# Performance work log

Hardware: AMD Instinct MI355X
Metric: run time of the kernel (lower is better)

Reference implementation:

```python
import jax, jax.numpy as jnp
import numpy as np

EPS = 1e-5
N_HEADS = 16
D_NOPE = 128
D_ROPE = 64
D_QK = D_NOPE + D_ROPE  # 192
D_V = 128
KV_RANK = 512
SCALE = D_QK ** -0.5


def rms_norm(x, w, eps=EPS):
    return x * jax.lax.rsqrt(jnp.mean(x * x, axis=-1, keepdims=True) + eps) * w


def apply_rope(x, c, s):
    # x: [..., D_ROPE], c/s broadcastable [..., D_ROPE//2]; half-split rotation
    x0, x1 = x[..., : D_ROPE // 2], x[..., D_ROPE // 2 :]
    return jnp.concatenate([x0 * c - x1 * s, x0 * s + x1 * c], axis=-1)


def setup_inputs() -> dict:
    key = jax.random.key(0)
    ks = jax.random.split(key, 8)
    B, S, H_DIM = 2, 2048, 2048
    Q_RANK = 1536
    w = lambda k, shp: jax.random.normal(k, shp, dtype=jnp.float32) * 0.02
    # real RoPE tables: [max_seq, D_ROPE//2]
    inv_freq = 1.0 / (10000.0 ** (np.arange(0, D_ROPE, 2, dtype=np.float32) / D_ROPE))
    ang = np.arange(S, dtype=np.float32)[:, None] * inv_freq[None, :]
    return {
        "x": jax.random.normal(ks[0], (B, S, H_DIM), dtype=jnp.float32),
        "positions": jnp.arange(S, dtype=jnp.int64),
        "Wqa": w(ks[1], (H_DIM, Q_RANK)),
        "g_qa": jnp.ones((Q_RANK,), jnp.float32),
        "Wqb": w(ks[2], (Q_RANK, N_HEADS * D_QK)),
        "Wkva": w(ks[3], (H_DIM, KV_RANK + D_ROPE)),
        "g_kva": jnp.ones((KV_RANK,), jnp.float32),
        "Wkvb": w(ks[4], (KV_RANK, N_HEADS * (D_NOPE + D_V))),
        "Wo": w(ks[5], (N_HEADS * D_V, H_DIM)),
        "cos": jnp.asarray(np.cos(ang)),
        "sin": jnp.asarray(np.sin(ang)),
    }


def reference(x, positions, Wqa, g_qa, Wqb, Wkva, g_kva, Wkvb, Wo, cos, sin):
    B, S, _ = x.shape
    # Q path: low-rank down, RMSNorm, up
    q = rms_norm(x @ Wqa, g_qa) @ Wqb  # [B,S,H*D_QK]
    q = q.reshape(B, S, N_HEADS, D_QK)
    q_nope, q_rope = q[..., :D_NOPE], q[..., D_NOPE:]
    c = cos[positions]  # [S, D_ROPE//2]
    s = sin[positions]
    q_rope = apply_rope(q_rope, c[None, :, None, :], s[None, :, None, :])
    # KV path: joint down-proj, split latent / rope-key
    kv_a = x @ Wkva  # [B,S,KV_RANK+D_ROPE]
    kv_latent = rms_norm(kv_a[..., :KV_RANK], g_kva)
    k_rope = apply_rope(kv_a[..., KV_RANK:], c[None, :, :], s[None, :, :])  # [B,S,D_ROPE]
    # up-project latent to per-head k_nope and v
    kv_b = (kv_latent @ Wkvb).reshape(B, S, N_HEADS, D_NOPE + D_V)
    k_nope, v = kv_b[..., :D_NOPE], kv_b[..., D_NOPE:]
    k = jnp.concatenate(
        [k_nope, jnp.broadcast_to(k_rope[:, :, None, :], (B, S, N_HEADS, D_ROPE))], axis=-1
    )  # [B,S,H,D_QK]
    q_full = jnp.concatenate([q_nope, q_rope], axis=-1)  # [B,S,H,D_QK]
    # causal SDPA with d_qk != d_v
    scores = jnp.einsum("bqhd,bkhd->bhqk", q_full, k) * SCALE
    causal = jnp.tril(jnp.ones((S, S), dtype=bool))
    scores = jnp.where(causal[None, None, :, :], scores, -jnp.inf)
    p = jax.nn.softmax(scores, axis=-1)
    out = jnp.einsum("bhqk,bkhd->bqhd", p, v).reshape(B, S, N_HEADS * D_V)
    return out @ Wo
```

## Files before the change

kernel.cpp:

```cpp
#include <hip/hip_runtime.h>
#include <hip/hip_bf16.h>

typedef __bf16 bf16;
typedef __bf16 bf16x8 __attribute__((ext_vector_type(8)));
typedef __bf16 bf16x4 __attribute__((ext_vector_type(4)));
typedef float f32x4 __attribute__((ext_vector_type(4)));

#define B_    2
#define S_    2048
#define HD    2048
#define NH    16
#define DQK   192
#define DV    128
#define QR    1536
#define KVR   512
#define NTOK  4096
#define NKVB  4096
#define NQB   3072
#define NQKVA 2176

#define EXP2F(x) __builtin_amdgcn_exp2f(x)

static __device__ __forceinline__ void gload16(const void* g, void* l) {
  __builtin_amdgcn_global_load_lds(
      (const __attribute__((address_space(1))) void*)g,
      (__attribute__((address_space(3))) void*)l, 16, 0, 0);
}

__global__ __launch_bounds__(256) void cvt_bf16(const float* __restrict__ in,
                                                bf16* __restrict__ out, long n) {
  long i = ((long)blockIdx.x * 256 + threadIdx.x) * 4;
  if (i + 3 < n) {
    float4 v = *(const float4*)(in + i);
    bf16x4 o = {(bf16)v.x, (bf16)v.y, (bf16)v.z, (bf16)v.w};
    *(bf16x4*)(out + i) = o;
  }
}

struct TransArgs {
  const float *s0, *s1, *s2, *s3, *s4;
  bf16 *d0, *d1, *d2, *d3, *d4;
};
__global__ __launch_bounds__(256) void transpose_all(TransArgs a) {
  __shared__ float tile[32][33];
  int bid = blockIdx.x;
  int seg, rel;
  if      (bid < 3072)  { seg = 0; rel = bid; }
  else if (bid < 4352)  { seg = 1; rel = bid - 3072; }
  else if (bid < 8960)  { seg = 2; rel = bid - 4352; }
  else if (bid < 11008) { seg = 3; rel = bid - 8960; }
  else                  { seg = 4; rel = bid - 11008; }
  const float* in = seg == 0 ? a.s0 : seg == 1 ? a.s1 : seg == 2 ? a.s2 : seg == 3 ? a.s3 : a.s4;
  bf16* out       = seg == 0 ? a.d0 : seg == 1 ? a.d1 : seg == 2 ? a.d2 : seg == 3 ? a.d3 : a.d4;
  int R   = seg == 0 ? 2048 : seg == 1 ? 2048 : seg == 2 ? 1536 : seg == 3 ? 512 : 2048;
  int C   = seg == 0 ? 1536 : seg == 1 ? 576  : seg == 2 ? 3072 : seg == 3 ? 4096 : 2048;
  int Np  = seg == 0 ? 1536 : seg == 1 ? 640  : seg == 2 ? 3072 : seg == 3 ? 4096 : 2048;
  int nbx = seg == 0 ? 48   : seg == 1 ? 20   : seg == 2 ? 96   : seg == 3 ? 128 : 64;
  int c0 = (rel % nbx) * 32;
  int r0 = (rel / nbx) * 32;
  int tx = threadIdx.x & 31, ty = threadIdx.x >> 5;
#pragma unroll
  for (int i = 0; i < 4; ++i) {
    int r = r0 + ty + i * 8, c = c0 + tx;
    tile[ty + i * 8][tx] = (c < C) ? in[(long)r * C + c] : 0.f;
  }
  __syncthreads();
#pragma unroll
  for (int i = 0; i < 4; ++i) {
    int oc = c0 + ty + i * 8;
    if (oc < Np) out[(long)oc * R + r0 + tx] = (bf16)tile[tx][ty + i * 8];
  }
}

#define GEMM_CORE(A, Bt, K)                                                    \
  __shared__ bf16 As[128 * 64];                                                \
  __shared__ bf16 Bs[128 * 64];                                                \
  const int t = threadIdx.x;                                                   \
  const int l = t & 63;                                                        \
  const int w = t >> 6;                                                        \
  const int m0 = blockIdx.y * 128;                                             \
  const int n0 = blockIdx.x * 128;                                             \
  const int wr = (w >> 1) * 64;                                                \
  const int wc = (w & 1) * 64;                                                 \
  const int lr = l & 15;                                                       \
  const int lg = l >> 4;                                                       \
  f32x4 acc[4][4] = {};                                                        \
  for (int k0 = 0; k0 < (K); k0 += 64) {                                       \
    __syncthreads();                                                           \
    _Pragma("unroll")                                                          \
    for (int j = 0; j < 4; ++j) {                                              \
      int s = j * 256 + t;                                                     \
      int row = s >> 3, sc = s & 7;                                            \
      int c = sc ^ (row & 7);                                                  \
      gload16((A) + (long)(m0 + row) * (K) + k0 + c * 8,                       \
              As + (j * 256 + w * 64) * 8);                                    \
      gload16((Bt) + (long)(n0 + row) * (K) + k0 + c * 8,                      \
              Bs + (j * 256 + w * 64) * 8);                                    \
    }                                                                          \
    __syncthreads();                                                           \
    _Pragma("unroll")                                                          \
    for (int kh = 0; kh < 2; ++kh) {                                           \
      bf16x8 af[4], bfr[4];                                                    \
      _Pragma("unroll")                                                        \
      for (int m = 0; m < 4; ++m) {                                            \
        int row = wr + m * 16 + lr;                                            \
        af[m] = *(const bf16x8*)(As + row * 64 + (((kh * 4 + lg) ^ (row & 7)) << 3)); \
      }                                                                        \
      _Pragma("unroll")                                                        \
      for (int n = 0; n < 4; ++n) {                                            \
        int row = wc + n * 16 + lr;                                            \
        bfr[n] = *(const bf16x8*)(Bs + row * 64 + (((kh * 4 + lg) ^ (row & 7)) << 3)); \
      }                                                                        \
      _Pragma("unroll")                                                        \
      for (int m = 0; m < 4; ++m)                                              \
        _Pragma("unroll")                                                      \
        for (int n = 0; n < 4; ++n)                                            \
          acc[m][n] = __builtin_amdgcn_mfma_f32_16x16x32_bf16(af[m], bfr[n], acc[m][n], 0, 0, 0); \
    }                                                                          \
  }

template <typename CT>
__global__ __launch_bounds__(256) void gemm_bf16(const bf16* __restrict__ A,
                                                 const bf16* __restrict__ Bt,
                                                 CT* __restrict__ C,
                                                 int M, int N, int K) {
  GEMM_CORE(A, Bt, K)
#pragma unroll
  for (int m = 0; m < 4; ++m)
#pragma unroll
    for (int n = 0; n < 4; ++n)
#pragma unroll
      for (int v = 0; v < 4; ++v) {
        int row = m0 + wr + m * 16 + lg * 4 + v;
        int col = n0 + wc + n * 16 + lr;
        C[(long)row * N + col] = (CT)acc[m][n][v];
      }
}

__global__ __launch_bounds__(256) void gemm_qf(const bf16* __restrict__ A,
                                               const bf16* __restrict__ Bt,
                                               const int* __restrict__ pos,
                                               const float* __restrict__ cosT,
                                               const float* __restrict__ sinT,
                                               bf16* __restrict__ q_bhsd) {
  const float SCALE = 0.07216878364870323f * 1.4426950408889634f;
  GEMM_CORE(A, Bt, QR)
  int c0 = n0 + wc;
  int h = c0 / 192;
  int part = c0 - h * 192;
#pragma unroll
  for (int m = 0; m < 4; ++m)
#pragma unroll
    for (int v = 0; v < 4; ++v) {
      int row = m0 + wr + m * 16 + lg * 4 + v;
      int b = row >> 11, s = row & (S_ - 1);
      long base = ((long)(b * NH + h) * S_ + s) * DQK;
      if (part < 128) {
#pragma unroll
        for (int n = 0; n < 4; ++n)
          q_bhsd[base + part + n * 16 + lr] = (bf16)(acc[m][n][v] * SCALE);
      } else {
        int p = pos[s] & (S_ - 1);
        float c_lo = cosT[p * 32 + lr],      s_lo = sinT[p * 32 + lr];
        float c_hi = cosT[p * 32 + 16 + lr], s_hi = sinT[p * 32 + 16 + lr];
        float o0 = acc[m][0][v] * c_lo - acc[m][2][v] * s_lo;
        float o1 = acc[m][1][v] * c_hi - acc[m][3][v] * s_hi;
        float o2 = acc[m][0][v] * s_lo + acc[m][2][v] * c_lo;
        float o3 = acc[m][1][v] * s_hi + acc[m][3][v] * c_hi;
        q_bhsd[base + 128 + lr] = (bf16)(o0 * SCALE);
        q_bhsd[base + 144 + lr] = (bf16)(o1 * SCALE);
        q_bhsd[base + 160 + lr] = (bf16)(o2 * SCALE);
        q_bhsd[base + 176 + lr] = (bf16)(o3 * SCALE);
      }
    }
}

__global__ __launch_bounds__(256) void gemm_kvb(const bf16* __restrict__ A,
                                                const bf16* __restrict__ Bt,
                                                bf16* __restrict__ k_bhsd,
                                                bf16* __restrict__ v_t) {
  GEMM_CORE(A, Bt, KVR)
  int c0 = n0 + wc;
  int h = c0 >> 8;
  int dbase = c0 & 64;
  bool vpart = (c0 >> 7) & 1;
  if (!vpart) {
#pragma unroll
    for (int m = 0; m < 4; ++m)
#pragma unroll
      for (int v = 0; v < 4; ++v) {
        int row = m0 + wr + m * 16 + lg * 4 + v;
        int b = row >> 11, s = row & (S_ - 1);
        long base = ((long)(b * NH + h) * S_ + s) * DQK + dbase;
#pragma unroll
        for (int n = 0; n < 4; ++n)
          k_bhsd[base + n * 16 + lr] = (bf16)acc[m][n][v];
      }
  } else {
#pragma unroll
    for (int m = 0; m < 4; ++m) {
      int row0 = m0 + wr + m * 16 + lg * 4;
      int b = row0 >> 11, s = row0 & (S_ - 1);
#pragma unroll
      for (int n = 0; n < 4; ++n) {
        int d = dbase + n * 16 + lr;
        bf16x4 o = {(bf16)acc[m][n][0], (bf16)acc[m][n][1],
                    (bf16)acc[m][n][2], (bf16)acc[m][n][3]};
        *(bf16x4*)(v_t + ((long)(b * NH + h) * DV + d) * S_ + s) = o;
      }
    }
  }
}

__global__ __launch_bounds__(256) void norm_prep(const bf16* __restrict__ xa,
                                                 const float* __restrict__ g_qa,
                                                 const float* __restrict__ g_kva,
                                                 const int* __restrict__ pos,
                                                 const float* __restrict__ cosT,
                                                 const float* __restrict__ sinT,
                                                 bf16* __restrict__ q_n,
                                                 bf16* __restrict__ kv_l,
                                                 bf16* __restrict__ k_bhsd) {
  int row = blockIdx.x;
  int t = threadIdx.x;
  int b = row >> 11, s = row & (S_ - 1);
  const bf16* xr = xa + (long)row * NQKVA;
  __shared__ float red[3];
  __shared__ bf16 rope_s[64];
  float vf[8];
  if (t < 192) {
    bf16x8 vv = *(const bf16x8*)(xr + t * 8);
    float ss = 0.f;
#pragma unroll
    for (int e = 0; e < 8; ++e) { vf[e] = (float)vv[e]; ss += vf[e] * vf[e]; }
#pragma unroll
    for (int m = 1; m < 64; m <<= 1) ss += __shfl_xor(ss, m);
    if ((t & 63) == 0) red[t >> 6] = ss;
  } else {
    int tt = t - 192;
    const bf16* xl = xr + QR;
    bf16x8 vv = *(const bf16x8*)(xl + tt * 8);
    float ss = 0.f;
#pragma unroll
    for (int e = 0; e < 8; ++e) { vf[e] = (float)vv[e]; ss += vf[e] * vf[e]; }
#pragma unroll
    for (int m = 1; m < 64; m <<= 1) ss += __shfl_xor(ss, m);
    float rs = rsqrtf(ss / KVR + 1e-5f);
    bf16x8 o;
#pragma unroll
    for (int e = 0; e < 8; ++e) o[e] = (bf16)(vf[e] * rs * g_kva[tt * 8 + e]);
    *(bf16x8*)(kv_l + (long)row * KVR + tt * 8) = o;
    if (tt < 32) {
      int p = pos[s] & (S_ - 1);
      float c = cosT[p * 32 + tt], sn = sinT[p * 32 + tt];
      float x0 = (float)xl[512 + tt], x1 = (float)xl[544 + tt];
      rope_s[tt] = (bf16)(x0 * c - x1 * sn);
      rope_s[32 + tt] = (bf16)(x0 * sn + x1 * c);
    }
  }
  __syncthreads();
  if (t < 192) {
    float ss = red[0] + red[1] + red[2];
    float rs = rsqrtf(ss / QR + 1e-5f);
    bf16x8 o;
#pragma unroll
    for (int e = 0; e < 8; ++e) o[e] = (bf16)(vf[e] * rs * g_qa[t * 8 + e]);
    *(bf16x8*)(q_n + (long)row * QR + t * 8) = o;
  } else {
    int tt = t - 192;
    bf16x8 rv = *(const bf16x8*)&rope_s[(tt & 7) * 8];
    long base0 = ((long)(b * NH + (tt >> 3)) * S_ + s) * DQK + 128 + (tt & 7) * 8;
    long base1 = ((long)(b * NH + 8 + (tt >> 3)) * S_ + s) * DQK + 128 + (tt & 7) * 8;
    *(bf16x8*)(k_bhsd + base0) = rv;
    *(bf16x8*)(k_bhsd + base1) = rv;
  }
}

#define KVB  64
#define DVP  144
__global__ __launch_bounds__(512) void flash4(const bf16* __restrict__ q_bhsd,
                                              const bf16* __restrict__ k_bhsd,
                                              const bf16* __restrict__ v_t,
                                              bf16* __restrict__ att) {
  __shared__ bf16 Ks[KVB * DQK];
  __shared__ bf16 Vs[DVP * KVB];
  __shared__ bf16 Ps[8][16 * 72];
  int bid = blockIdx.x;
  int bh = bid & 31;
  int qt = 15 - (bid >> 5);
  int b = bh >> 4, h = bh & 15;
  int q0 = qt * 128;
  int t = threadIdx.x;
  int w = t >> 6, l = t & 63;
  int lr = l & 15, lg = l >> 4;
  int qw = q0 + w * 16;

  const bf16* Qb = q_bhsd + (long)bh * S_ * DQK;
  const bf16* Kb = k_bhsd + (long)bh * S_ * DQK;
  const bf16* Vb = v_t + (long)bh * DV * S_;

  if (t < 128) {
    int rr = 128 + (t >> 3), cc = (t & 7) * 8;
    bf16 val = (bf16)((rr == 128) ? 1.0f : 0.0f);
    bf16x8 vvv = {val, val, val, val, val, val, val, val};
    *(bf16x8*)(Vs + rr * KVB + cc) = vvv;
  }

  bf16x8 qf[6];
#pragma unroll
  for (int t6 = 0; t6 < 6; ++t6)
    qf[t6] = *(const bf16x8*)(Qb + (long)(qw + lr) * DQK + t6 * 32 + lg * 8);

  f32x4 oacc[9] = {};
  float mrow[4] = {-1e30f, -1e30f, -1e30f, -1e30f};
  const int lr7 = lr & 7;

  int nkt = 2 * qt + 2;
  for (int kt = 0; kt < nkt; ++kt) {
    int k0 = kt * KVB;
    __syncthreads();
#pragma unroll
    for (int j = 0; j < 3; ++j) {
      int s = j * 512 + t;
      int r = s / 24, c1 = s - r * 24;
      int c = c1 ^ (r & 7);
      gload16(Kb + (long)(k0 + r) * DQK + c * 8, Ks + (j * 512 + w * 64) * 8);
    }
#pragma unroll
    for (int j = 0; j < 2; ++j) {
      int s = j * 512 + t;
      int d = s >> 3, c1 = s & 7;
      int c = c1 ^ (d & 7);
      gload16(Vb + (long)d * S_ + k0 + c * 8, Vs + (j * 512 + w * 64) * 8);
    }
    __syncthreads();
    if (k0 > qw + 15) continue;

    f32x4 sacc[4] = {};
#pragma unroll
    for (int n = 0; n < 4; ++n) {
      int rk = n * 16 + lr;
#pragma unroll
      for (int t6 = 0; t6 < 6; ++t6) {
        bf16x8 kf = *(const bf16x8*)(Ks + rk * DQK + (((t6 * 4 + lg) ^ lr7) << 3));
        sacc[n] = __builtin_amdgcn_mfma_f32_16x16x32_bf16(qf[t6], kf, sacc[n], 0, 0, 0);
      }
    }
    if (k0 + KVB - 1 > qw) {
#pragma unroll
      for (int n = 0; n < 4; ++n)
#pragma unroll
        for (int v = 0; v < 4; ++v) {
          int r = lg * 4 + v, c = n * 16 + lr;
          if (k0 + c > qw + r) sacc[n][v] = -1e30f;
        }
    }
    float mv[4];
#pragma unroll
    for (int v = 0; v < 4; ++v) {
      mv[v] = fmaxf(fmaxf(sacc[0][v], sacc[1][v]), fmaxf(sacc[2][v], sacc[3][v]));
#pragma unroll
      for (int msk = 1; msk < 16; msk <<= 1) mv[v] = fmaxf(mv[v], __shfl_xor(mv[v], msk));
    }
    bool grow = (mv[0] > mrow[0] + 8.f) | (mv[1] > mrow[1] + 8.f) |
                (mv[2] > mrow[2] + 8.f) | (mv[3] > mrow[3] + 8.f);
    if (__any(grow)) {
      float corr[4];
#pragma unroll
      for (int v = 0; v < 4; ++v) {
        float mt = fmaxf(mrow[v], mv[v]);
        corr[v] = EXP2F(mrow[v] - mt);
        mrow[v] = mt;
      }
#pragma unroll
      for (int dn = 0; dn < 9; ++dn)
#pragma unroll
        for (int v = 0; v < 4; ++v) oacc[dn][v] *= corr[v];
    }
#pragma unroll
    for (int v = 0; v < 4; ++v)
#pragma unroll
      for (int n = 0; n < 4; ++n)
        Ps[w][(lg * 4 + v) * 72 + n * 16 + lr] = (bf16)EXP2F(sacc[n][v] - mrow[v]);
#pragma unroll
    for (int kc = 0; kc < 2; ++kc) {
      bf16x8 pf = *(const bf16x8*)(Ps[w] + lr * 72 + kc * 32 + lg * 8);
#pragma unroll
      for (int dn = 0; dn < 9; ++dn) {
        int d = dn * 16 + lr;
        bf16x8 vf = *(const bf16x8*)(Vs + d * KVB + (((kc * 4 + lg) ^ lr7) << 3));
        oacc[dn] = __builtin_amdgcn_mfma_f32_16x16x32_bf16(pf, vf, oacc[dn], 0, 0, 0);
      }
    }
  }
  float rl[4];
#pragma unroll
  for (int v = 0; v < 4; ++v) {
    float lv = __shfl(oacc[8][v], lg * 16);
    rl[v] = 1.0f / lv;
  }
#pragma unroll
  for (int dn = 0; dn < 8; ++dn)
#pragma unroll
    for (int v = 0; v < 4; ++v) {
      int r = lg * 4 + v;
      float o = oacc[dn][v] * rl[v];
      att[((long)(b * S_ + qw + r)) * 2048 + h * 128 + dn * 16 + lr] = (bf16)o;
    }
}

extern "C" void kernel_launch(void* const* d_in, const int* in_sizes, int n_in,
                              void* d_out, int out_size, void* d_ws, size_t ws_size,
                              hipStream_t stream) {
  const float* x        = (const float*)d_in[0];
  const int* pos        = (const int*)d_in[1];
  const float* Wqa      = (const float*)d_in[2];
  const float* g_qa     = (const float*)d_in[3];
  const float* Wqb      = (const float*)d_in[4];
  const float* Wkva     = (const float*)d_in[5];
  const float* g_kva    = (const float*)d_in[6];
  const float* Wkvb     = (const float*)d_in[7];
  const float* Wo       = (const float*)d_in[8];
  const float* cosT     = (const float*)d_in[9];
  const float* sinT     = (const float*)d_in[10];
  float* out            = (float*)d_out;

  size_t off = 0;
  char* wsp = (char*)d_ws;
  auto alloc = [&](size_t n) { void* p = wsp + off; off += (n + 255) & ~(size_t)255; return p; };
  bf16*  Wqa_t  = (bf16*) alloc((size_t)QR * HD * 2);
  bf16*  Wkva_t = (bf16*) alloc((size_t)640 * HD * 2);
  bf16*  Wqb_t  = (bf16*) alloc((size_t)NQB * QR * 2);
  bf16*  Wkvb_t = (bf16*) alloc((size_t)NKVB * KVR * 2);
  bf16*  Wo_t   = (bf16*) alloc((size_t)HD * HD * 2);
  bf16*  x_bf   = (bf16*) alloc((size_t)NTOK * HD * 2);
  bf16*  q_bhsd = (bf16*) alloc((size_t)B_ * NH * S_ * DQK * 2);
  bf16*  k_bhsd = (bf16*) alloc((size_t)B_ * NH * S_ * DQK * 2);
  bf16*  v_t    = (bf16*) alloc((size_t)B_ * NH * DV * S_ * 2);
  bf16*  att    = (bf16*) alloc((size_t)NTOK * 2048 * 2);
  char*  T      = (char*) alloc((size_t)33554432);
  bf16*  xa  = (bf16*)T;
  bf16*  q_n = (bf16*)(T + 18874368);
  bf16*  kv_l = (bf16*)(T + 18874368 + 12582912);
  if (ws_size < off) return;

  cvt_bf16<<<(NTOK * HD / 4 + 255) / 256, 256, 0, stream>>>(x, x_bf, (long)NTOK * HD);
  TransArgs ta = {Wqa, Wkva, Wqb, Wkvb, Wo, Wqa_t, Wkva_t, Wqb_t, Wkvb_t, Wo_t};
  transpose_all<<<15104, 256, 0, stream>>>(ta);
  gemm_bf16<bf16><<<dim3(NQKVA / 128, NTOK / 128), 256, 0, stream>>>(x_bf, Wqa_t, xa, NTOK, NQKVA, HD);
  norm_prep<<<NTOK, 256, 0, stream>>>(xa, g_qa, g_kva, pos, cosT, sinT, q_n, kv_l, k_bhsd);
  gemm_qf<<<dim3(NQB / 128, NTOK / 128), 256, 0, stream>>>(q_n, Wqb_t, pos, cosT, sinT, q_bhsd);
  gemm_kvb<<<dim3(NKVB / 128, NTOK / 128), 256, 0, stream>>>(kv_l, Wkvb_t, k_bhsd, v_t);
  flash4<<<512, 512, 0, stream>>>(q_bhsd, k_bhsd, v_t, att);
  gemm_bf16<float><<<dim3(HD / 128, NTOK / 128), 256, 0, stream>>>(att, Wo_t, out, NTOK, HD, HD);
}
```

Before: 320.1 us.

## Use 256x256-tile 8-wave pipelined GEMM for Q and KV up-projections

Replaces the 128x128 GEMM core used by the Q up-projection and KV up-projection kernels with a new 256x256-tile, 512-thread core. The new core double-buffers LDS with async global-to-LDS loads, XOR-swizzles LDS rows, and interleaves next-tile prefetch with MFMA groups under raised wave priority. Larger tiles raise data reuse and the pipelining hides load latency. In exchange, each GEMM launches fewer blocks (e.g. 192 and 256), which may underfill the GPU, and LDS use and register pressure are higher.

```diff
diff --git a/kernel.cpp b/kernel.cpp
--- a/kernel.cpp
+++ b/kernel.cpp
@@ -137,36 +137,119 @@
       }
 }
 
-__global__ __launch_bounds__(256) void gemm_qf(const bf16* __restrict__ A,
-                                               const bf16* __restrict__ Bt,
-                                               const int* __restrict__ pos,
-                                               const float* __restrict__ cosT,
-                                               const float* __restrict__ sinT,
-                                               bf16* __restrict__ q_bhsd) {
+#define G8P_CORE(A, Bt, K)                                                     \
+  __shared__ bf16 As_[2][256 * 64];                                            \
+  __shared__ bf16 Bs_[2][256 * 64];                                            \
+  const int t = threadIdx.x;                                                   \
+  const int w = t >> 6, l = t & 63;                                            \
+  const int lr = l & 15, lg = l >> 4;                                          \
+  const int wm = w >> 2, wn = w & 3;                                           \
+  const int m0 = blockIdx.y * 256, n0 = blockIdx.x * 256;                      \
+  const int NT = (K) >> 6;                                                     \
+  const int tr = t >> 3, sc = t & 7;                                           \
+  f32x4 acc[8][4] = {};                                                        \
+  auto stg = [&](int kt, int j) {                                              \
+    int jj = j & 3;                                                            \
+    int row = jj * 64 + tr;                                                    \
+    int c = sc ^ (row & 7);                                                    \
+    const bf16* src = (j < 4)                                                  \
+        ? (A)  + (long)(m0 + row) * (K) + kt * 64 + c * 8                      \
+        : (Bt) + (long)(n0 + row) * (K) + kt * 64 + c * 8;                     \
+    bf16* dst = ((j < 4) ? As_[kt & 1] : Bs_[kt & 1]) + (jj * 512 + w * 64) * 8; \
+    gload16(src, dst);                                                         \
+  };                                                                           \
+  _Pragma("unroll") for (int j = 0; j < 8; ++j) stg(0, j);                     \
+  _Pragma("unroll") for (int j = 0; j < 8; ++j) stg(1, j);                     \
+  for (int kt = 0; kt < NT; ++kt) {                                            \
+    const bf16* Ab = As_[kt & 1];                                              \
+    const bf16* Bb = Bs_[kt & 1];                                              \
+    if (kt == NT - 1) { asm volatile("s_waitcnt vmcnt(0)" ::: "memory"); }     \
+    else              { asm volatile("s_waitcnt vmcnt(8)" ::: "memory"); }     \
+    __builtin_amdgcn_s_barrier();                                              \
+    asm volatile("" ::: "memory");                                             \
+    bf16x8 af[8][2], bfr[4][2];                                                \
+    _Pragma("unroll")                                                          \
+    for (int mi = 0; mi < 8; ++mi) {                                           \
+      int row = wm * 128 + mi * 16 + lr;                                       \
+      _Pragma("unroll")                                                        \
+      for (int kh = 0; kh < 2; ++kh)                                           \
+        af[mi][kh] = *(const bf16x8*)(Ab + row * 64 + (((kh * 4 + lg) ^ (row & 7)) << 3)); \
+    }                                                                          \
+    _Pragma("unroll")                                                          \
+    for (int ni = 0; ni < 4; ++ni) {                                           \
+      int row = wn * 64 + ni * 16 + lr;                                        \
+      _Pragma("unroll")                                                        \
+      for (int kh = 0; kh < 2; ++kh)                                           \
+        bfr[ni][kh] = *(const bf16x8*)(Bb + row * 64 + (((kh * 4 + lg) ^ (row & 7)) << 3)); \
+    }                                                                          \
+    asm volatile("s_waitcnt lgkmcnt(0)" ::: "memory");                         \
+    __builtin_amdgcn_sched_barrier(0);                                         \
+    __builtin_amdgcn_s_setprio(1);                                             \
+    _Pragma("unroll")                                                          \
+    for (int mi = 0; mi < 8; ++mi)                                             \
+      _Pragma("unroll")                                                        \
+      for (int kh = 0; kh < 2; ++kh)                                           \
+        acc[mi][0] = __builtin_amdgcn_mfma_f32_16x16x32_bf16(af[mi][kh], bfr[0][kh], acc[mi][0], 0, 0, 0); \
+    __builtin_amdgcn_s_setprio(0);                                             \
+    __builtin_amdgcn_s_barrier();    \
+    asm volatile("" ::: "memory");                                             \
+    bool more = (kt + 2) < NT;                                                 \
+    if (more) { stg(kt + 2, 0); stg(kt + 2, 1); stg(kt + 2, 2); }              \
+    __builtin_amdgcn_s_setprio(1);                                             \
+    _Pragma("unroll")                                                          \
+    for (int mi = 0; mi < 8; ++mi)                                             \
+      _Pragma("unroll")                                                        \
+      for (int kh = 0; kh < 2; ++kh)                                           \
+        acc[mi][1] = __builtin_amdgcn_mfma_f32_16x16x32_bf16(af[mi][kh], bfr[1][kh], acc[mi][1], 0, 0, 0); \
+    __builtin_amdgcn_s_setprio(0);                                             \
+    if (more) { stg(kt + 2, 3); stg(kt + 2, 4); stg(kt + 2, 5); }              \
+    __builtin_amdgcn_s_setprio(1);                                             \
+    _Pragma("unroll")                                                          \
+    for (int mi = 0; mi < 8; ++mi)                                             \
+      _Pragma("unroll")                                                        \
+      for (int kh = 0; kh < 2; ++kh)                                           \
+        acc[mi][2] = __builtin_amdgcn_mfma_f32_16x16x32_bf16(af[mi][kh], bfr[2][kh], acc[mi][2], 0, 0, 0); \
+    __builtin_amdgcn_s_setprio(0);                                             \
+    if (more) { stg(kt + 2, 6); stg(kt + 2, 7); }                              \
+    __builtin_amdgcn_s_setprio(1);                                             \
+    _Pragma("unroll")                                                          \
+    for (int mi = 0; mi < 8; ++mi)                                             \
+      _Pragma("unroll")                                                        \
+      for (int kh = 0; kh < 2; ++kh)                                           \
+        acc[mi][3] = __builtin_amdgcn_mfma_f32_16x16x32_bf16(af[mi][kh], bfr[3][kh], acc[mi][3], 0, 0, 0); \
+    __builtin_amdgcn_s_setprio(0);                                             \
+  }
+
+__global__ __launch_bounds__(512) void gemm8p_qf(const bf16* __restrict__ A,
+                                                 const bf16* __restrict__ Bt,
+                                                 const int* __restrict__ pos,
+                                                 const float* __restrict__ cosT,
+                                                 const float* __restrict__ sinT,
+                                                 bf16* __restrict__ q_bhsd) {
   const float SCALE = 0.07216878364870323f * 1.4426950408889634f;
-  GEMM_CORE(A, Bt, QR)
-  int c0 = n0 + wc;
+  G8P_CORE(A, Bt, QR)
+  int c0 = n0 + wn * 64;
   int h = c0 / 192;
   int part = c0 - h * 192;
 #pragma unroll
-  for (int m = 0; m < 4; ++m)
+  for (int mi = 0; mi < 8; ++mi)
 #pragma unroll
     for (int v = 0; v < 4; ++v) {
-      int row = m0 + wr + m * 16 + lg * 4 + v;
+      int row = m0 + wm * 128 + mi * 16 + lg * 4 + v;
       int b = row >> 11, s = row & (S_ - 1);
       long base = ((long)(b * NH + h) * S_ + s) * DQK;
       if (part < 128) {
 #pragma unroll
-        for (int n = 0; n < 4; ++n)
-          q_bhsd[base + part + n * 16 + lr] = (bf16)(acc[m][n][v] * SCALE);
+        for (int ni = 0; ni < 4; ++ni)
+          q_bhsd[base + part + ni * 16 + lr] = (bf16)(acc[mi][ni][v] * SCALE);
       } else {
         int p = pos[s] & (S_ - 1);
         float c_lo = cosT[p * 32 + lr],      s_lo = sinT[p * 32 + lr];
         float c_hi = cosT[p * 32 + 16 + lr], s_hi = sinT[p * 32 + 16 + lr];
-        float o0 = acc[m][0][v] * c_lo - acc[m][2][v] * s_lo;
-        float o1 = acc[m][1][v] * c_hi - acc[m][3][v] * s_hi;
-        float o2 = acc[m][0][v] * s_lo + acc[m][2][v] * c_lo;
-        float o3 = acc[m][1][v] * s_hi + acc[m][3][v] * c_hi;
+        float o0 = acc[mi][0][v] * c_lo - acc[mi][2][v] * s_lo;
+        float o1 = acc[mi][1][v] * c_hi - acc[mi][3][v] * s_hi;
+        float o2 = acc[mi][0][v] * s_lo + acc[mi][2][v] * c_lo;
+        float o3 = acc[mi][1][v] * s_hi + acc[mi][3][v] * c_hi;
         q_bhsd[base + 128 + lr] = (bf16)(o0 * SCALE);
         q_bhsd[base + 144 + lr] = (bf16)(o1 * SCALE);
         q_bhsd[base + 160 + lr] = (bf16)(o2 * SCALE);
@@ -175,37 +258,37 @@
     }
 }
 
-__global__ __launch_bounds__(256) void gemm_kvb(const bf16* __restrict__ A,
-                                                const bf16* __restrict__ Bt,
-                                                bf16* __restrict__ k_bhsd,
-                                                bf16* __restrict__ v_t) {
-  GEMM_CORE(A, Bt, KVR)
-  int c0 = n0 + wc;
+__global__ __launch_bounds__(512) void gemm8p_kvb(const bf16* __restrict__ A,
+                                                  const bf16* __restrict__ Bt,
+                                                  bf16* __restrict__ k_bhsd,
+                                                  bf16* __restrict__ v_t) {
+  G8P_CORE(A, Bt, KVR)
+  int c0 = n0 + wn * 64;
   int h = c0 >> 8;
   int dbase = c0 & 64;
   bool vpart = (c0 >> 7) & 1;
   if (!vpart) {
 #pragma unroll
-    for (int m = 0; m < 4; ++m)
+    for (int mi = 0; mi < 8; ++mi)
 #pragma unroll
       for (int v = 0; v < 4; ++v) {
-        int row = m0 + wr + m * 16 + lg * 4 + v;
+        int row = m0 + wm * 128 + mi * 16 + lg * 4 + v;
         int b = row >> 11, s = row & (S_ - 1);
         long base = ((long)(b * NH + h) * S_ + s) * DQK + dbase;
 #pragma unroll
-        for (int n = 0; n < 4; ++n)
-          k_bhsd[base + n * 16 + lr] = (bf16)acc[m][n][v];
+        for (int ni = 0; ni < 4; ++ni)
+          k_bhsd[base + ni * 16 + lr] = (bf16)acc[mi][ni][v];
       }
   } else {
 #pragma unroll
-    for (int m = 0; m < 4; ++m) {
-      int row0 = m0 + wr + m * 16 + lg * 4;
+    for (int mi = 0; mi < 8; ++mi) {
+      int row0 = m0 + wm * 128 + mi * 16 + lg * 4;
       int b = row0 >> 11, s = row0 & (S_ - 1);
 #pragma unroll
-      for (int n = 0; n < 4; ++n) {
-        int d = dbase + n * 16 + lr;
-        bf16x4 o = {(bf16)acc[m][n][0], (bf16)acc[m][n][1],
-                    (bf16)acc[m][n][2], (bf16)acc[m][n][3]};
+      for (int ni = 0; ni < 4; ++ni) {
+        int d = dbase + ni * 16 + lr;
+        bf16x4 o = {(bf16)acc[mi][ni][0], (bf16)acc[mi][ni][1],
+                    (bf16)acc[mi][ni][2], (bf16)acc[mi][ni][3]};
         *(bf16x4*)(v_t + ((long)(b * NH + h) * DV + d) * S_ + s) = o;
       }
     }
@@ -449,8 +532,8 @@
   transpose_all<<<15104, 256, 0, stream>>>(ta);
   gemm_bf16<bf16><<<dim3(NQKVA / 128, NTOK / 128), 256, 0, stream>>>(x_bf, Wqa_t, xa, NTOK, NQKVA, HD);
   norm_prep<<<NTOK, 256, 0, stream>>>(xa, g_qa, g_kva, pos, cosT, sinT, q_n, kv_l, k_bhsd);
-  gemm_qf<<<dim3(NQB / 128, NTOK / 128), 256, 0, stream>>>(q_n, Wqb_t, pos, cosT, sinT, q_bhsd);
-  gemm_kvb<<<dim3(NKVB / 128, NTOK / 128), 256, 0, stream>>>(kv_l, Wkvb_t, k_bhsd, v_t);
+  gemm8p_qf<<<dim3(NQB / 256, NTOK / 256), 512, 0, stream>>>(q_n, Wqb_t, pos, cosT, sinT, q_bhsd);
+  gemm8p_kvb<<<dim3(NKVB / 256, NTOK / 256), 512, 0, stream>>>(kv_l, Wkvb_t, k_bhsd, v_t);
   flash4<<<512, 512, 0, stream>>>(q_bhsd, k_bhsd, v_t, att);
   gemm_bf16<float><<<dim3(HD / 128, NTOK / 128), 256, 0, stream>>>(att, Wo_t, out, NTOK, HD, HD);
 }
```

After: 298.1 us. -6.9%, faster.
